# Performance work log

Measured on AMD Instinct MI355X. Metric: run time of the kernel, lower is better.

Reference implementation:

```python
import jax, jax.numpy as jnp
import numpy as np

BETA = 0.9       # leak factor (snn.Leaky beta)
THRESH = 1.0     # default snn.Leaky threshold
ALPHA = 2.0      # default ATan surrogate alpha

@jax.custom_vjp
def atan_spike(x):
    # Heaviside forward, ATan surrogate backward (snntorch default spike_grad)
    return (x > 0).astype(x.dtype)

def _atan_fwd(x):
    return (x > 0).astype(x.dtype), x

def _atan_bwd(x, g):
    # d/dx ~ (alpha/2) / (1 + (pi/2 * alpha * x)^2)
    return (g * (ALPHA / 2) / (1 + (jnp.pi / 2 * ALPHA * x) ** 2),)

atan_spike.defvjp(_atan_fwd, _atan_bwd)

def setup_inputs() -> dict:
    key = jax.random.key(0)
    k1, k2 = jax.random.split(key)
    B, IN, OUT, T = 64, 1024, 1024, 256
    x = jax.random.normal(k1, (B, IN, T), dtype=jnp.float32)
    W = jax.random.normal(k2, (OUT, IN), dtype=jnp.float32) * (1.0 / np.sqrt(IN))
    return {"x": x, "W": W}

def reference(x, W):
    # Batch all per-timestep GEMMs into one contraction: syn[b,o,t]
    syn = jnp.einsum('bit,oi->bot', x, W)
    syn_t = jnp.moveaxis(syn, -1, 0)  # [T, B, OUT]
    mem0 = jnp.zeros(syn.shape[:-1], syn.dtype)  # [B, OUT]

    def step(mem, s):
        # snntorch Leaky (subtract reset): reset from previous mem (detached),
        # then state update, then spike from new mem.
        reset = jax.lax.stop_gradient((mem > THRESH).astype(mem.dtype))
        mem = BETA * mem + s - reset * THRESH
        spk = atan_spike(mem - THRESH)
        return mem, spk

    _, spks = jax.lax.scan(step, mem0, syn_t)  # spks: [T, B, OUT]
    return jnp.moveaxis(spks, 0, -1)  # [B, OUT, T]
```

## Files before the change

kernel.cpp:

```cpp
#include <hip/hip_runtime.h>


#define B_DIM 64
#define IN_DIM 1024
#define OUT_DIM 1024
#define T_DIM 256

typedef int v4i __attribute__((ext_vector_type(4)));
typedef int v16i __attribute__((ext_vector_type(16)));
typedef double v4d __attribute__((ext_vector_type(4)));

#define LO_OFF   0ull
#define WSL_OFF  67108864ull
#define XSL_OFF  73400320ull
#define AL_OFF   174063616ull
#define BE_OFF   174067712ull
#define PART_OFF 174133248ull
#define WS_NEED  175181824ull

__device__ __forceinline__ void gload_lds16(const void* g, void* l)
{
    __builtin_amdgcn_global_load_lds(
        (const __attribute__((address_space(1))) void*)g,
        (__attribute__((address_space(3))) void*)l, 16, 0, 0);
}

__device__ __forceinline__ void dig4_extract(unsigned bits, int bem,
                                             signed char* d )
{
    const int be = (bits >> 23) & 255;
    unsigned M = (bits & 0x7fffffu) | (be ? 0x800000u : 0u);
    const int sh = be - bem + 4;
    unsigned fix = 0;
    if (sh >= 0) fix = M << sh;
    else if (sh > -32) fix = M >> (-sh);
    int d0 = (fix >> 21) & 127, d1 = (fix >> 14) & 127,
        d2 = (fix >> 7) & 127,  d3 = fix & 127;
    if (bits & 0x80000000u) { d0 = -d0; d1 = -d1; d2 = -d2; d3 = -d3; }
    d[0] = (signed char)d0; d[1] = (signed char)d1;
    d[2] = (signed char)d2; d[3] = (signed char)d3;
}

__global__ __launch_bounds__(256) void k_aux_wx(
    const float* __restrict__ W, signed char* __restrict__ wsl,
    int* __restrict__ alpha_e,
    const float* __restrict__ x, float* __restrict__ part)
{
    __shared__ float red[256];
    __shared__ float wrow[1024];
    __shared__ int se;
    __shared__ float4 bp[4][64];
    const int tid = threadIdx.x;

    if (blockIdx.x < 1024) {
        const int o = blockIdx.x;
        float4 v = *(const float4*)&W[(size_t)o * IN_DIM + tid * 4];
        *(float4*)&wrow[tid * 4] = v;
        float m = fmaxf(fmaxf(fabsf(v.x), fabsf(v.y)), fmaxf(fabsf(v.z), fabsf(v.w)));
        red[tid] = m; __syncthreads();
        for (int s = 128; s > 0; s >>= 1) {
            if (tid < s) red[tid] = fmaxf(red[tid], red[tid + s]);
            __syncthreads();
        }
        if (tid == 0) { int e = 0; if (red[0] > 0.f) frexpf(red[0], &e); se = e; alpha_e[o] = e; }
        __syncthreads();
        if (tid >= 64) return;
        const int bem = se + 126;
        const int ks = tid >> 1, khalf = tid & 1;
        const int k0 = tid * 16;
        const int lane = (o & 31) + 32 * khalf;

        signed char dig[16][4];
        #pragma unroll
        for (int j = 0; j < 16; ++j)
            dig4_extract(__float_as_uint(wrow[k0 + j]), bem, dig[j]);

        #pragma unroll
        for (int p = 0; p < 4; ++p) {
            int w[4];
            #pragma unroll
            for (int g = 0; g < 4; ++g)
                w[g] = (dig[4*g][p] & 0xff) | ((dig[4*g+1][p] & 0xff) << 8) |
                       ((dig[4*g+2][p] & 0xff) << 16) | ((dig[4*g+3][p] & 0xff) << 24);
            const size_t base =
                (((size_t)p * 32 + (o >> 5)) * 32 + ks) * 1024 + lane * 16;
            *(v4i*)&wsl[base] = (v4i){w[0], w[1], w[2], w[3]};
        }
    } else {
        const int idx = blockIdx.x - 1024;
        const int ic = idx & 15, b = idx >> 4;
        const int quarter = tid >> 6, t4 = (tid & 63) * 4;
        const float* p = x + ((size_t)b * IN_DIM + ic * 64 + quarter * 16) * T_DIM + t4;
        float4 m4 = make_float4(0.f, 0.f, 0.f, 0.f);
        #pragma unroll
        for (int r = 0; r < 16; ++r) {
            float4 v = *(const float4*)&p[(size_t)r * T_DIM];
            m4.x = fmaxf(m4.x, fabsf(v.x)); m4.y = fmaxf(m4.y, fabsf(v.y));
            m4.z = fmaxf(m4.z, fabsf(v.z)); m4.w = fmaxf(m4.w, fabsf(v.w));
        }
        bp[quarter][tid & 63] = m4;
        __syncthreads();
        if (tid < 64) {
            float4 a = bp[0][tid], b4 = bp[1][tid], c = bp[2][tid], d = bp[3][tid];
            float4 r;
            r.x = fmaxf(fmaxf(a.x, b4.x), fmaxf(c.x, d.x));
            r.y = fmaxf(fmaxf(a.y, b4.y), fmaxf(c.y, d.y));
            r.z = fmaxf(fmaxf(a.z, b4.z), fmaxf(c.z, d.z));
            r.w = fmaxf(fmaxf(a.w, b4.w), fmaxf(c.w, d.w));
            *(float4*)&part[((size_t)b * 16 + ic) * T_DIM + tid * 4] = r;
        }
    }
}

__global__ __launch_bounds__(256) void k_beta(const float* __restrict__ part,
                                              int* __restrict__ beta_e)
{
    const int b = blockIdx.x, t = threadIdx.x;
    float m = 0.f;
    #pragma unroll
    for (int ic = 0; ic < 16; ++ic)
        m = fmaxf(m, part[((size_t)b * 16 + ic) * T_DIM + t]);
    int e = 0;
    if (m > 0.f) frexpf(m, &e);
    beta_e[b * T_DIM + t] = e;
}

__global__ __launch_bounds__(256) void k_slice_x(const float* __restrict__ x,
    const int* __restrict__ beta_e, signed char* __restrict__ xsl)
{
    __shared__ float ft[64][68];
    const int tb = blockIdx.x;
    const int ib = blockIdx.y;
    const int b  = blockIdx.z;
    const int tid = threadIdx.x;
    const int t0 = tb * 64, i0 = ib * 64;
    #pragma unroll
    for (int p = 0; p < 4; ++p) {
        int id4 = tid + p * 256;
        int il = id4 >> 4, c4 = (id4 & 15) * 4;
        float4 v = *(const float4*)&x[((size_t)b * IN_DIM + i0 + il) * T_DIM + t0 + c4];
        *(float4*)&ft[il][c4] = v;
    }
    __syncthreads();

    const int t32l = tid >> 7;
    const int ksl  = (tid >> 6) & 1;
    const int lane = tid & 63;
    const int t_local = t32l * 32 + (lane & 31);
    const int k_local = ksl * 32 + (lane >> 5) * 16;
    const int e = beta_e[b * T_DIM + t0 + t_local];
    const int bem = e + 126;

    signed char dig[16][4];
    #pragma unroll
    for (int j = 0; j < 16; ++j)
        dig4_extract(__float_as_uint(ft[k_local + j][t_local]), bem, dig[j]);

    #pragma unroll
    for (int p = 0; p < 4; ++p) {
        int w[4];
        #pragma unroll
        for (int g = 0; g < 4; ++g)
            w[g] = (dig[4*g][p] & 0xff) | ((dig[4*g+1][p] & 0xff) << 8) |
                   ((dig[4*g+2][p] & 0xff) << 16) | ((dig[4*g+3][p] & 0xff) << 24);
        const size_t base =
            ((((size_t)p * B_DIM + b) * 8 + (tb * 2 + t32l)) * 32 + (ib * 2 + ksl)) * 1024
            + lane * 16;
        *(v4i*)&xsl[base] = (v4i){w[0], w[1], w[2], w[3]};
    }
}

#define OZ_LOADS(PF)                                                        \
    {                                                                       \
        _Pragma("unroll")                                                   \
        for (int j = 0; j < 5; ++j) {                                       \
            gload_lds16(gp[j], &LB[PF][lbase + j * 8192]);                  \
            gp[j] += 1024;                                                  \
        }                                                                   \
    }

#define OZ_MATH(CUR)                                                        \
    {                                                                       \
        const signed char* base_ = LB[CUR];                                 \
        v4i af[4];                                                          \
        _Pragma("unroll")                                                   \
        for (int p = 0; p < 4; ++p)                                         \
            af[p] = *(const v4i*)(base_ + p * 2048 + aoffm);                \
        __builtin_amdgcn_s_setprio(1);                                      \
        _Pragma("unroll")                                                   \
        for (int q = 0; q < 4; ++q) {                                       \
            v4i b0 = *(const v4i*)(base_ + q * 8192 + boffm);               \
            v4i b1 = *(const v4i*)(base_ + q * 8192 + boffm + 1024);        \
            _Pragma("unroll")                                               \
            for (int p = 0; p + q < 4; ++p) {                               \
                accA[p + q] = __builtin_amdgcn_mfma_i32_32x32x32_i8(        \
                    af[p], b0, accA[p + q], 0, 0, 0);                       \
                accB[p + q] = __builtin_amdgcn_mfma_i32_32x32x32_i8(        \
                    af[p], b1, accB[p + q], 0, 0, 0);                       \
            }                                                               \
        }                                                                   \
        __builtin_amdgcn_s_setprio(0);                                      \
    }

#define VMBAR(N)                                                            \
    do {                                                                    \
        asm volatile("s_waitcnt vmcnt(" #N ")" ::: "memory");               \
        __builtin_amdgcn_s_barrier();                                       \
    } while (0)

__global__ __launch_bounds__(512, 2) void k_oz_gemm_fused(
    const signed char* __restrict__ wsl, const signed char* __restrict__ xsl,
    const int* __restrict__ alpha_e, const int* __restrict__ beta_e,
    float* __restrict__ out)
{
    __shared__ __align__(16) signed char LB[3][40960];

    const int tid = threadIdx.x;
    const int lane = tid & 63, wave = tid >> 6;
    const int bid = blockIdx.x;
    const int ob = bid >> 6;
    const int rr = bid & 63;
    const int b  = ((rr & 7) << 3) + (rr >> 3);
    const int o0 = ob * 64;
    const int woh = wave >> 2;
    const int wtq = wave & 3;
    const int l16 = lane * 16;

    v16i accA[4], accB[4];
    #pragma unroll
    for (int s = 0; s < 4; ++s) {
        accA[s] = (v16i){0,0,0,0,0,0,0,0,0,0,0,0,0,0,0,0};
        accB[s] = (v16i){0,0,0,0,0,0,0,0,0,0,0,0,0,0,0,0};
    }

    const signed char* gp[5];
    #pragma unroll
    for (int j = 0; j < 5; ++j) {
        const int s = 8 * j + wave;
        if (s < 8) {
            gp[j] = wsl + ((size_t)(s >> 1) << 20)
                        + ((size_t)(2 * ob + (s & 1)) << 15) + l16;
        } else {
            const int u = s - 8;
            gp[j] = xsl + ((size_t)(u >> 3) << 24) + ((size_t)b << 18)
                        + ((size_t)(u & 7) << 15) + l16;
        }
    }
    const int lbase = wave * 1024;

    const int aoffm = woh * 1024 + l16;
    const int boffm = 8192 + wtq * 2048 + l16;

    OZ_LOADS(0)
    OZ_LOADS(1)
    VMBAR(5);

    #pragma unroll 1
    for (int it = 0; it < 10; ++it) {
        OZ_LOADS(2) OZ_MATH(0) VMBAR(5);
        OZ_LOADS(0) OZ_MATH(1) VMBAR(5);
        OZ_LOADS(1) OZ_MATH(2) VMBAR(5);
    }
    OZ_MATH(0) VMBAR(0);
    OZ_MATH(1)

    const int lr = lane & 31;
    const int rv = (lr + 1) * 0x01010101;
    const v4i pav  = {rv, rv, rv, rv};
    const v4i onev = {0x01010101, 0x01010101, 0x01010101, 0x01010101};
    const v16i z = (v16i){0,0,0,0,0,0,0,0,0,0,0,0,0,0,0,0};
    v16i d1 = __builtin_amdgcn_mfma_i32_32x32x32_i8(pav, onev, z, 0, 0, 0);
    v16i d2 = __builtin_amdgcn_mfma_i32_32x32x32_i8(onev, pav, z, 0, 0, 0);

    const int col = (d2[0] >> 5) - 1;
    const int gtA = wtq * 64 + col;
    const int gtB = gtA + 32;
    const int ebA = beta_e[b * T_DIM + gtA];
    const int ebB = beta_e[b * T_DIM + gtB];

    const double C0 = 0x1p-14, C1 = 0x1p-21, C2 = 0x1p-28, C3 = 0x1p-35;
    double synA_[16], synB_[16];
    int go_[16];
    #pragma unroll
    for (int r = 0; r < 16; ++r) {
        const int row = (d1[r] >> 5) - 1;
        const int go = woh * 32 + row;
        go_[r] = go;
        const int ea = alpha_e[o0 + go];
        double vA = (double)accA[0][r] * C0 + (double)accA[1][r] * C1 +
                    (double)accA[2][r] * C2 + (double)accA[3][r] * C3;
        double vB = (double)accB[0][r] * C0 + (double)accB[1][r] * C1 +
                    (double)accB[2][r] * C2 + (double)accB[3][r] * C3;
        synA_[r] = ldexp(vA, ea + ebA);
        synB_[r] = ldexp(vB, ea + ebB);
    }

    double* synbuf = (double*)&LB[0][0];
    float*  spkbuf = (float*)&LB[1][0];
    float*  outp = out + ((size_t)b * OUT_DIM + o0) * T_DIM;
    double mem = 0.0;

    __syncthreads();
    #pragma unroll 1
    for (int c = 0; c < 4; ++c) {
        if (wtq == c) {
            #pragma unroll
            for (int r = 0; r < 16; ++r) {
                synbuf[(size_t)col * 65 + go_[r]]        = synA_[r];
                synbuf[(size_t)(col + 32) * 65 + go_[r]] = synB_[r];
            }
        }
        __syncthreads();
        if (wave == 0) {
            float sp[64];
            #pragma unroll
            for (int g = 0; g < 4; ++g) {
                double sv[16];
                #pragma unroll
                for (int k = 0; k < 16; ++k)
                    sv[k] = synbuf[(size_t)(g * 16 + k) * 65 + lane];
                #pragma unroll
                for (int k = 0; k < 16; ++k) {
                    double a = 0.9 * mem + sv[k];
                    mem = (mem > 1.0) ? (a - 1.0) : a;
                    sp[g * 16 + k] = (mem > 1.0) ? 1.0f : 0.0f;
                }
            }
            #pragma unroll
            for (int k4 = 0; k4 < 16; ++k4)
                *(float4*)&spkbuf[lane * 68 + k4 * 4] = make_float4(
                    sp[k4 * 4], sp[k4 * 4 + 1], sp[k4 * 4 + 2], sp[k4 * 4 + 3]);
        }
        __syncthreads();
        {
            const int o = tid >> 3, tg = tid & 7;
            float4 v0 = *(float4*)&spkbuf[o * 68 + tg * 8];
            float4 v1 = *(float4*)&spkbuf[o * 68 + tg * 8 + 4];
            float* dst = outp + (size_t)o * T_DIM + c * 64 + tg * 8;
            *(float4*)&dst[0] = v0;
            *(float4*)&dst[4] = v1;
        }
        __syncthreads();
    }
}

#define BM 128
#define BN 128
#define BK 16
#define LDA 130

__global__ __launch_bounds__(256, 2) void spk_gemm_mfma64p_kernel(
    const float* __restrict__ x, const float* __restrict__ W,
    float* __restrict__ syn_hi, float* __restrict__ syn_lo)
{
    const int tid  = threadIdx.x;
    const int lane = tid & 63;
    const int wave = tid >> 6;
    const int tb = blockIdx.x, ob = blockIdx.y, b = blockIdx.z;

    __shared__ __align__(16) double As[BK][LDA];
    __shared__ __align__(16) double Bs[BK][LDA];

    const v4d zz = {0.0, 0.0, 0.0, 0.0};
    v4d d1 = __builtin_amdgcn_mfma_f64_16x16x4f64((double)lane, 1.0, zz, 0, 0, 0);
    v4d d2 = __builtin_amdgcn_mfma_f64_16x16x4f64(1.0, (double)lane, zz, 0, 0, 0);
    const bool a_h1 = (((int)d1[0] & 3) == 0);
    const bool b_h1 = (((int)d2[0] & 3) == 0);
    int drow[4];
    #pragma unroll
    for (int r = 0; r < 4; ++r) {
        const int v = (int)d1[r];
        drow[r] = (a_h1 ? (v - 96) >> 2 : (v - 6) >> 4) & 15;
    }
    const int am = a_h1 ? (lane & 15) : (lane >> 2);
    const int ak = a_h1 ? (lane >> 4) : (lane & 3);
    const int bn = b_h1 ? (lane & 15) : (lane >> 2);
    const int bk = b_h1 ? (lane >> 4) : (lane & 3);
    const int dcol = lane & 15;

    const int o0 = ob * BM, t0 = tb * BN;
    const float* Wp = W + (size_t)o0 * IN_DIM;
    const float* xp = x + (size_t)b * IN_DIM * T_DIM + t0;
    const int wo = (wave >> 1) * 64, wt = (wave & 1) * 64;

    v4d acc[4][4];
    #pragma unroll
    for (int i = 0; i < 4; ++i)
        #pragma unroll
        for (int j = 0; j < 4; ++j) acc[i][j] = zz;

    const int ar0 = tid / 4, ac = (tid % 4) * 4;
    const int bkr0 = tid / 32, btc = (tid % 32) * 4;

    float4 pa[2], pb[2];
    #pragma unroll
    for (int p = 0; p < 2; ++p) {
        pa[p] = *(const float4*)&Wp[(size_t)(ar0 + p * 64) * IN_DIM + ac];
        pb[p] = *(const float4*)&xp[(size_t)(bkr0 + p * 8) * T_DIM + btc];
    }

    for (int k0 = 0; k0 < IN_DIM; k0 += BK) {
        #pragma unroll
        for (int p = 0; p < 2; ++p) {
            const int r = ar0 + p * 64;
            As[ac + 0][r] = (double)pa[p].x; As[ac + 1][r] = (double)pa[p].y;
            As[ac + 2][r] = (double)pa[p].z; As[ac + 3][r] = (double)pa[p].w;
            const int kr = bkr0 + p * 8;
            Bs[kr][btc + 0] = (double)pb[p].x; Bs[kr][btc + 1] = (double)pb[p].y;
            Bs[kr][btc + 2] = (double)pb[p].z; Bs[kr][btc + 3] = (double)pb[p].w;
        }
        if (k0 + BK < IN_DIM) {
            #pragma unroll
            for (int p = 0; p < 2; ++p) {
                pa[p] = *(const float4*)&Wp[(size_t)(ar0 + p * 64) * IN_DIM + k0 + BK + ac];
                pb[p] = *(const float4*)&xp[(size_t)(bkr0 + p * 8 + k0 + BK) * T_DIM + btc];
            }
        }
        __syncthreads();
        #pragma unroll
        for (int kk = 0; kk < 4; ++kk) {
            const int kra = kk * 4 + ak, krb = kk * 4 + bk;
            double a[4], bb[4];
            #pragma unroll
            for (int i = 0; i < 4; ++i) a[i] = As[kra][wo + i * 16 + am];
            #pragma unroll
            for (int j = 0; j < 4; ++j) bb[j] = Bs[krb][wt + j * 16 + bn];
            #pragma unroll
            for (int i = 0; i < 4; ++i)
                #pragma unroll
                for (int j = 0; j < 4; ++j)
                    acc[i][j] = __builtin_amdgcn_mfma_f64_16x16x4f64(a[i], bb[j], acc[i][j], 0, 0, 0);
        }
        __syncthreads();
    }

    float* ohi = syn_hi + ((size_t)b * OUT_DIM + o0) * T_DIM + t0;
    float* olo = syn_lo + ((size_t)b * OUT_DIM + o0) * T_DIM + t0;
    #pragma unroll
    for (int i = 0; i < 4; ++i)
        #pragma unroll
        for (int j = 0; j < 4; ++j) {
            const int col = wt + j * 16 + dcol;
            #pragma unroll
            for (int r = 0; r < 4; ++r) {
                double s = acc[i][j][r];
                float hi = (float)s;
                float lo = (float)(s - (double)hi);
                const size_t off = (size_t)(wo + i * 16 + drow[r]) * T_DIM + col;
                ohi[off] = hi; olo[off] = lo;
            }
        }
}

__global__ __launch_bounds__(256) void spk_scan_f64_kernel(
    float* __restrict__ hi, const float* __restrict__ lo)
{
    const int TC = 16;
    __shared__ float thi[256][TC + 1];
    __shared__ float tlo[256][TC + 1];
    const int tid = threadIdx.x;
    const size_t row0 = (size_t)blockIdx.x * 256;

    double mem = 0.0;
    for (int t0 = 0; t0 < T_DIM; t0 += TC) {
        #pragma unroll
        for (int p = 0; p < 4; ++p) {
            int id = tid + p * 256;
            int r = id / 4, c = (id % 4) * 4;
            size_t g = (row0 + r) * T_DIM + t0 + c;
            float4 vh = *(const float4*)&hi[g];
            thi[r][c] = vh.x; thi[r][c+1] = vh.y; thi[r][c+2] = vh.z; thi[r][c+3] = vh.w;
            float4 vl = *(const float4*)&lo[g];
            tlo[r][c] = vl.x; tlo[r][c+1] = vl.y; tlo[r][c+2] = vl.z; tlo[r][c+3] = vl.w;
        }
        __syncthreads();
        float spk[TC];
        #pragma unroll
        for (int t = 0; t < TC; ++t) {
            double s = (double)thi[tid][t] + (double)tlo[tid][t];
            double reset = (mem > 1.0) ? 1.0 : 0.0;
            mem = 0.9 * mem + s - reset;
            spk[t] = ((mem - 1.0) > 0.0) ? 1.0f : 0.0f;
        }
        __syncthreads();
        #pragma unroll
        for (int t = 0; t < TC; ++t) thi[tid][t] = spk[t];
        __syncthreads();
        #pragma unroll
        for (int p = 0; p < 4; ++p) {
            int id = tid + p * 256;
            int r = id / 4, c = (id % 4) * 4;
            float4 v = make_float4(thi[r][c], thi[r][c+1], thi[r][c+2], thi[r][c+3]);
            *(float4*)&hi[(row0 + r) * T_DIM + t0 + c] = v;
        }
        __syncthreads();
    }
}

extern "C" void kernel_launch(void* const* d_in, const int* in_sizes, int n_in,
                              void* d_out, int out_size, void* d_ws, size_t ws_size,
                              hipStream_t stream)
{
    const float* x = (const float*)d_in[0];
    const float* W = (const float*)d_in[1];
    float* hi = (float*)d_out;
    char* ws = (char*)d_ws;
    float* lo = (float*)(ws + LO_OFF);

    if (ws_size >= WS_NEED) {
        signed char* wsl = (signed char*)(ws + WSL_OFF);
        signed char* xsl = (signed char*)(ws + XSL_OFF);
        int* alpha = (int*)(ws + AL_OFF);
        int* beta  = (int*)(ws + BE_OFF);
        float* part = (float*)(ws + PART_OFF);

        k_aux_wx<<<dim3(2048), dim3(256), 0, stream>>>(W, wsl, alpha, x, part);
        k_beta<<<dim3(B_DIM), dim3(256), 0, stream>>>(part, beta);
        k_slice_x<<<dim3(4, 16, B_DIM), dim3(256), 0, stream>>>(x, beta, xsl);
        k_oz_gemm_fused<<<dim3(1024), dim3(512), 0, stream>>>(wsl, xsl, alpha, beta, hi);
    } else {
        spk_gemm_mfma64p_kernel<<<dim3(2, 8, B_DIM), dim3(256), 0, stream>>>(x, W, hi, lo);
        spk_scan_f64_kernel<<<dim3((B_DIM * OUT_DIM) / 256), dim3(256), 0, stream>>>(hi, lo);
    }
}
```

Baseline: 306.9 us.

## Fuse beta exponent into slice kernel and widen GEMM wave tiles to 256 threads

Removes the separate k_beta launch by computing the per-timestep exponent inside k_slice_x from the partial maxima, with only ib==0 blocks writing it out for the GEMM. The int8 Ozaki GEMM changes from 8 waves to 4 waves per block, and each wave now covers both 32-row output halves, doubling its accumulators so each B fragment read from LDS feeds twice as many MFMAs. The aim is less LDS traffic per MFMA and one fewer launch. The cost is much higher register pressure (16 v16i accumulators) and fewer waves per CU, with each wave issuing 10 global-to-LDS loads per stage.

```diff
diff --git a/kernel.cpp b/kernel.cpp
--- a/kernel.cpp
+++ b/kernel.cpp
@@ -112,23 +112,12 @@
     }
 }
 
-__global__ __launch_bounds__(256) void k_beta(const float* __restrict__ part,
-                                              int* __restrict__ beta_e)
-{
-    const int b = blockIdx.x, t = threadIdx.x;
-    float m = 0.f;
-    #pragma unroll
-    for (int ic = 0; ic < 16; ++ic)
-        m = fmaxf(m, part[((size_t)b * 16 + ic) * T_DIM + t]);
-    int e = 0;
-    if (m > 0.f) frexpf(m, &e);
-    beta_e[b * T_DIM + t] = e;
-}
-
 __global__ __launch_bounds__(256) void k_slice_x(const float* __restrict__ x,
-    const int* __restrict__ beta_e, signed char* __restrict__ xsl)
+    const float* __restrict__ part, int* __restrict__ beta_e,
+    signed char* __restrict__ xsl)
 {
     __shared__ float ft[64][68];
+    __shared__ int se_arr[64];
     const int tb = blockIdx.x;
     const int ib = blockIdx.y;
     const int b  = blockIdx.z;
@@ -141,6 +130,17 @@
         float4 v = *(const float4*)&x[((size_t)b * IN_DIM + i0 + il) * T_DIM + t0 + c4];
         *(float4*)&ft[il][c4] = v;
     }
+    if (tid < 64) {
+        const int t = t0 + tid;
+        float m = 0.f;
+        #pragma unroll
+        for (int ic = 0; ic < 16; ++ic)
+            m = fmaxf(m, part[((size_t)b * 16 + ic) * T_DIM + t]);
+        int e = 0;
+        if (m > 0.f) frexpf(m, &e);
+        se_arr[tid] = e;
+        if (ib == 0) beta_e[b * T_DIM + t] = e;
+    }
     __syncthreads();
 
     const int t32l = tid >> 7;
@@ -148,8 +148,7 @@
     const int lane = tid & 63;
     const int t_local = t32l * 32 + (lane & 31);
     const int k_local = ksl * 32 + (lane >> 5) * 16;
-    const int e = beta_e[b * T_DIM + t0 + t_local];
-    const int bem = e + 126;
+    const int bem = se_arr[t_local] + 126;
 
     signed char dig[16][4];
     #pragma unroll
@@ -173,8 +172,8 @@
 #define OZ_LOADS(PF)                                                        \
     {                                                                       \
         _Pragma("unroll")                                                   \
-        for (int j = 0; j < 5; ++j) {                                       \
-            gload_lds16(gp[j], &LB[PF][lbase + j * 8192]);                  \
+        for (int j = 0; j < 10; ++j) {                                      \
+            gload_lds16(gp[j], &LB[PF][lbase + j * 4096]);                  \
             gp[j] += 1024;                                                  \
         }                                                                   \
     }
@@ -182,22 +181,26 @@
 #define OZ_MATH(CUR)                                                        \
     {                                                                       \
         const signed char* base_ = LB[CUR];                                 \
-        v4i af[4];                                                          \
+        v4i af[4][2];                                                       \
         _Pragma("unroll")                                                   \
         for (int p = 0; p < 4; ++p)                                         \
-            af[p] = *(const v4i*)(base_ + p * 2048 + aoffm);                \
+            _Pragma("unroll")                                               \
+            for (int os = 0; os < 2; ++os)                                  \
+                af[p][os] = *(const v4i*)(base_ + p * 2048 + os * 1024 + l16); \
         __builtin_amdgcn_s_setprio(1);                                      \
         _Pragma("unroll")                                                   \
         for (int q = 0; q < 4; ++q) {                                       \
-            v4i b0 = *(const v4i*)(base_ + q * 8192 + boffm);               \
-            v4i b1 = *(const v4i*)(base_ + q * 8192 + boffm + 1024);        \
+            v4i b0 = *(const v4i*)(base_ + 8192 + q * 8192 + t32a * 1024 + l16); \
+            v4i b1 = *(const v4i*)(base_ + 8192 + q * 8192 + t32a * 1024 + 1024 + l16); \
             _Pragma("unroll")                                               \
-            for (int p = 0; p + q < 4; ++p) {                               \
-                accA[p + q] = __builtin_amdgcn_mfma_i32_32x32x32_i8(        \
-                    af[p], b0, accA[p + q], 0, 0, 0);                       \
-                accB[p + q] = __builtin_amdgcn_mfma_i32_32x32x32_i8(        \
-                    af[p], b1, accB[p + q], 0, 0, 0);                       \
-            }                                                               \
+            for (int p = 0; p + q < 4; ++p)                                 \
+                _Pragma("unroll")                                           \
+                for (int os = 0; os < 2; ++os) {                            \
+                    accA[os][p + q] = __builtin_amdgcn_mfma_i32_32x32x32_i8( \
+                        af[p][os], b0, accA[os][p + q], 0, 0, 0);           \
+                    accB[os][p + q] = __builtin_amdgcn_mfma_i32_32x32x32_i8( \
+                        af[p][os], b1, accB[os][p + q], 0, 0, 0);           \
+                }                                                           \
         }                                                                   \
         __builtin_amdgcn_s_setprio(0);                                      \
     }
@@ -208,7 +211,7 @@
         __builtin_amdgcn_s_barrier();                                       \
     } while (0)
 
-__global__ __launch_bounds__(512, 2) void k_oz_gemm_fused(
+__global__ __launch_bounds__(256, 1) void k_oz_gemm_fused(
     const signed char* __restrict__ wsl, const signed char* __restrict__ xsl,
     const int* __restrict__ alpha_e, const int* __restrict__ beta_e,
     float* __restrict__ out)
@@ -222,21 +225,22 @@
     const int rr = bid & 63;
     const int b  = ((rr & 7) << 3) + (rr >> 3);
     const int o0 = ob * 64;
-    const int woh = wave >> 2;
-    const int wtq = wave & 3;
+    const int t32a = 2 * wave;
     const int l16 = lane * 16;
 
-    v16i accA[4], accB[4];
-    #pragma unroll
-    for (int s = 0; s < 4; ++s) {
-        accA[s] = (v16i){0,0,0,0,0,0,0,0,0,0,0,0,0,0,0,0};
-        accB[s] = (v16i){0,0,0,0,0,0,0,0,0,0,0,0,0,0,0,0};
-    }
-
-    const signed char* gp[5];
-    #pragma unroll
-    for (int j = 0; j < 5; ++j) {
-        const int s = 8 * j + wave;
+    v16i accA[2][4], accB[2][4];
+    #pragma unroll
+    for (int os = 0; os < 2; ++os)
+        #pragma unroll
+        for (int s = 0; s < 4; ++s) {
+            accA[os][s] = (v16i){0,0,0,0,0,0,0,0,0,0,0,0,0,0,0,0};
+            accB[os][s] = (v16i){0,0,0,0,0,0,0,0,0,0,0,0,0,0,0,0};
+        }
+
+    const signed char* gp[10];
+    #pragma unroll
+    for (int j = 0; j < 10; ++j) {
+        const int s = 4 * j + wave;
         if (s < 8) {
             gp[j] = wsl + ((size_t)(s >> 1) << 20)
                         + ((size_t)(2 * ob + (s & 1)) << 15) + l16;
@@ -248,18 +252,15 @@
     }
     const int lbase = wave * 1024;
 
-    const int aoffm = woh * 1024 + l16;
-    const int boffm = 8192 + wtq * 2048 + l16;
-
     OZ_LOADS(0)
     OZ_LOADS(1)
-    VMBAR(5);
+    VMBAR(10);
 
     #pragma unroll 1
     for (int it = 0; it < 10; ++it) {
-        OZ_LOADS(2) OZ_MATH(0) VMBAR(5);
-        OZ_LOADS(0) OZ_MATH(1) VMBAR(5);
-        OZ_LOADS(1) OZ_MATH(2) VMBAR(5);
+        OZ_LOADS(2) OZ_MATH(0) VMBAR(10);
+        OZ_LOADS(0) OZ_MATH(1) VMBAR(10);
+        OZ_LOADS(1) OZ_MATH(2) VMBAR(10);
     }
     OZ_MATH(0) VMBAR(0);
     OZ_MATH(1)
@@ -273,26 +274,28 @@
     v16i d2 = __builtin_amdgcn_mfma_i32_32x32x32_i8(onev, pav, z, 0, 0, 0);
 
     const int col = (d2[0] >> 5) - 1;
-    const int gtA = wtq * 64 + col;
+    const int gtA = wave * 64 + col;
     const int gtB = gtA + 32;
     const int ebA = beta_e[b * T_DIM + gtA];
     const int ebB = beta_e[b * T_DIM + gtB];
 
     const double C0 = 0x1p-14, C1 = 0x1p-21, C2 = 0x1p-28, C3 = 0x1p-35;
-    double synA_[16], synB_[16];
-    int go_[16];
+    double synA_[2][16], synB_[2][16];
+    int row_[16];
     #pragma unroll
     for (int r = 0; r < 16; ++r) {
-        const int row = (d1[r] >> 5) - 1;
-        const int go = woh * 32 + row;
-        go_[r] = go;
-        const int ea = alpha_e[o0 + go];
-        double vA = (double)accA[0][r] * C0 + (double)accA[1][r] * C1 +
-                    (double)accA[2][r] * C2 + (double)accA[3][r] * C3;
-        double vB = (double)accB[0][r] * C0 + (double)accB[1][r] * C1 +
-                    (double)accB[2][r] * C2 + (double)accB[3][r] * C3;
-        synA_[r] = ldexp(vA, ea + ebA);
-        synB_[r] = ldexp(vB, ea + ebB);
+        row_[r] = (d1[r] >> 5) - 1;
+        #pragma unroll
+        for (int os = 0; os < 2; ++os) {
+            const int go = os * 32 + row_[r];
+            const int ea = alpha_e[o0 + go];
+            double vA = (double)accA[os][0][r] * C0 + (double)accA[os][1][r] * C1 +
+                        (double)accA[os][2][r] * C2 + (double)accA[os][3][r] * C3;
+            double vB = (double)accB[os][0][r] * C0 + (double)accB[os][1][r] * C1 +
+                        (double)accB[os][2][r] * C2 + (double)accB[os][3][r] * C3;
+            synA_[os][r] = ldexp(vA, ea + ebA);
+            synB_[os][r] = ldexp(vB, ea + ebB);
+        }
     }
 
     double* synbuf = (double*)&LB[0][0];
@@ -303,12 +306,15 @@
     __syncthreads();
     #pragma unroll 1
     for (int c = 0; c < 4; ++c) {
-        if (wtq == c) {
-            #pragma unroll
-            for (int r = 0; r < 16; ++r) {
-                synbuf[(size_t)col * 65 + go_[r]]        = synA_[r];
-                synbuf[(size_t)(col + 32) * 65 + go_[r]] = synB_[r];
-            }
+        if (wave == c) {
+            #pragma unroll
+            for (int r = 0; r < 16; ++r)
+                #pragma unroll
+                for (int os = 0; os < 2; ++os) {
+                    const int go = os * 32 + row_[r];
+                    synbuf[(size_t)col * 65 + go]        = synA_[os][r];
+                    synbuf[(size_t)(col + 32) * 65 + go] = synB_[os][r];
+                }
         }
         __syncthreads();
         if (wave == 0) {
@@ -333,12 +339,13 @@
         }
         __syncthreads();
         {
-            const int o = tid >> 3, tg = tid & 7;
-            float4 v0 = *(float4*)&spkbuf[o * 68 + tg * 8];
-            float4 v1 = *(float4*)&spkbuf[o * 68 + tg * 8 + 4];
-            float* dst = outp + (size_t)o * T_DIM + c * 64 + tg * 8;
-            *(float4*)&dst[0] = v0;
-            *(float4*)&dst[4] = v1;
+            const int o = tid >> 2, tg = tid & 3;
+            float* dst = outp + (size_t)o * T_DIM + c * 64;
+            #pragma unroll
+            for (int k = 0; k < 4; ++k) {
+                float4 v = *(float4*)&spkbuf[o * 68 + tg * 16 + k * 4];
+                *(float4*)&dst[tg * 16 + k * 4] = v;
+            }
         }
         __syncthreads();
     }
@@ -515,9 +522,8 @@
         float* part = (float*)(ws + PART_OFF);
 
         k_aux_wx<<<dim3(2048), dim3(256), 0, stream>>>(W, wsl, alpha, x, part);
-        k_beta<<<dim3(B_DIM), dim3(256), 0, stream>>>(part, beta);
-        k_slice_x<<<dim3(4, 16, B_DIM), dim3(256), 0, stream>>>(x, beta, xsl);
-        k_oz_gemm_fused<<<dim3(1024), dim3(512), 0, stream>>>(wsl, xsl, alpha, beta, hi);
+        k_slice_x<<<dim3(4, 16, B_DIM), dim3(256), 0, stream>>>(x, part, beta, xsl);
+        k_oz_gemm_fused<<<dim3(1024), dim3(256), 0, stream>>>(wsl, xsl, alpha, beta, hi);
     } else {
         spk_gemm_mfma64p_kernel<<<dim3(2, 8, B_DIM), dim3(256), 0, stream>>>(x, W, hi, lo);
         spk_scan_f64_kernel<<<dim3((B_DIM * OUT_DIM) / 256), dim3(256), 0, stream>>>(hi, lo);
```

Result: slower. 320.1 us (+4.3%).
